# Performance work log

Hardware: AMD Instinct MI355X
Metric: run time of the kernel (lower is better)

Reference implementation:

```python
import jax, jax.numpy as jnp
import numpy as np

BS, SL, N_AGENTS, OBS_DIM, STATE_DIM, N_EDGES, HID = 32, 512, 32, 96, 1024, 64, 256


def _hgcn(w_line, x, H):
    # x: [B, n, 1]; H: [B, n, E]. Faithful to torch HGCN:
    # A = D^{-1/2} H |W| B^{-1} H^T D^{-1/2}, with D, B built from detached H/|W|,
    # inf entries (from 0^{-1} / 0^{-0.5}) zeroed. Diagonal matmuls are implicit scalings.
    w_abs = jnp.abs(w_line)
    Hd = jax.lax.stop_gradient(H)
    d = jnp.einsum('bne,e->bn', Hd, jax.lax.stop_gradient(w_abs))  # [B, n]
    d_is = jnp.where(d > 0, jax.lax.rsqrt(jnp.where(d > 0, d, 1.0)), 0.0)
    b = jnp.sum(Hd, axis=-2)  # [B, E]
    b_inv = jnp.where(b > 0, 1.0 / jnp.where(b > 0, b, 1.0), 0.0)
    t = d_is[..., None] * x                       # D^{-1/2} x
    s = jnp.einsum('bne,bnk->bek', H, t)          # H^T (...)
    s = s * (w_abs[None, :] * b_inv)[..., None]   # |W| B^{-1} (diagonals commute)
    y = jnp.einsum('bne,bek->bnk', H, s)          # H (...)
    return d_is[..., None] * y                    # D^{-1/2} (...)


def _mlp(x, w1, b1, w2, b2):
    return jax.nn.relu(x @ w1 + b1) @ w2 + b2


def setup_inputs() -> dict:
    key = jax.random.key(0)
    ks = jax.random.split(key, 24)
    f = jax.random.normal
    inp = {
        'agent_qs': f(ks[0], (BS, SL, N_AGENTS), jnp.float32),
        'states': f(ks[1], (BS, SL, STATE_DIM), jnp.float32),
        'indiv_us': f(ks[2], (BS, SL, N_AGENTS, OBS_DIM), jnp.float32),
        'edge_W': f(ks[3], (OBS_DIM, N_EDGES), jnp.float32) * 0.1,
        'edge_b': f(ks[4], (N_EDGES,), jnp.float32) * 0.1,
        'wline1': 1.0 + 0.1 * f(ks[5], (N_EDGES,), jnp.float32),
        'wline2': 1.0 + 0.1 * f(ks[6], (N_EDGES,), jnp.float32),
    }
    names = ['hw1', 'hc1', 'hw', 'hc']
    outs = [N_AGENTS, N_AGENTS, N_AGENTS, 1]
    for i, (nm, od) in enumerate(zip(names, outs)):
        inp[nm + '_w1'] = f(ks[7 + 4 * i], (STATE_DIM, HID), jnp.float32) * 0.05
        inp[nm + '_b1'] = f(ks[8 + 4 * i], (HID,), jnp.float32) * 0.05
        inp[nm + '_w2'] = f(ks[9 + 4 * i], (HID, od), jnp.float32) * 0.05
        inp[nm + '_b2'] = f(ks[10 + 4 * i], (od,), jnp.float32) * 0.05
    return inp


def reference(agent_qs, states, indiv_us, edge_W, edge_b, wline1, wline2,
              hw1_w1, hw1_b1, hw1_w2, hw1_b2, hc1_w1, hc1_b1, hc1_w2, hc1_b2,
              hw_w1, hw_b1, hw_w2, hw_b2, hc_w1, hc_b1, hc_w2, hc_b2):
    bs, sl, n = agent_qs.shape
    q = agent_qs.reshape(-1, n)                               # [B, n]
    u = indiv_us.reshape(-1, n, indiv_us.shape[-1])           # [B, n, obs]
    s = states.reshape(-1, states.shape[-1])                  # [B, state_dim]
    H = jax.nn.relu(u @ edge_W + edge_b)                      # hyper_edge_net -> [B, n, E]
    x = q[..., None]                                          # node_features [B, n, 1]
    qs_tot = _hgcn(wline2, _hgcn(wline1, x, H), H)[..., 0]    # two stacked HGCN encoders
    w1 = jnp.abs(_mlp(s, hw1_w1, hw1_b1, hw1_w2, hw1_b2))
    c1 = _mlp(s, hc1_w1, hc1_b1, hc1_w2, hc1_b2)
    qt = jax.nn.elu(qs_tot * w1 + c1)
    w = jnp.abs(_mlp(s, hw_w1, hw_b1, hw_w2, hw_b2))
    c = _mlp(s, hc_w1, hc_b1, hc_w2, hc_b2)[..., 0]
    q_tot = jnp.sum(qt * w, axis=-1) + c
    return q_tot.reshape(bs, sl, 1)
```

## Files before the change

### kernel.cpp

```cpp
#include <hip/hip_runtime.h>
#include <cstdint>

typedef _Float16 f16;
typedef _Float16 f16x2 __attribute__((ext_vector_type(2)));
typedef _Float16 f16x4 __attribute__((ext_vector_type(4)));
typedef _Float16 f16x8 __attribute__((ext_vector_type(8)));
typedef float f32x4 __attribute__((ext_vector_type(4)));

#define AS1U const __attribute__((address_space(1))) unsigned int
#define AS3U __attribute__((address_space(3))) unsigned int

__device__ __forceinline__ void gload_lds16(const void* g, void* l) {
    __builtin_amdgcn_global_load_lds((AS1U*)g, (AS3U*)l, 16, 0, 0);
}

#define WSYNC() asm volatile("s_waitcnt lgkmcnt(0)" ::: "memory")

#define BATCH 16384
#define NAG   32
#define OBS   96
#define SDIM  1024
#define NE    64
#define HIDN  256
#define NH    1024

#define NB_ST 1024
#define NB_PW 256
#define NB_SM 101
#define NB_HG 4096
#define NB_FRONT (NB_ST + NB_PW + NB_SM + NB_HG)

__global__ __launch_bounds__(256) void k_front(
    const float* __restrict__ agent_qs, const float* __restrict__ states,
    const float* __restrict__ indiv_us, const float* __restrict__ edge_W,
    const float* __restrict__ edge_b, const float* __restrict__ wline1,
    const float* __restrict__ wline2,
    const float* __restrict__ w1a, const float* __restrict__ w1b,
    const float* __restrict__ w1c, const float* __restrict__ w1d,
    const float* __restrict__ b1a, const float* __restrict__ b1b,
    const float* __restrict__ b1c, const float* __restrict__ b1d,
    const float* __restrict__ w2a, const float* __restrict__ w2b,
    const float* __restrict__ w2c, const float* __restrict__ w2d,
    f16* __restrict__ states16, f16* __restrict__ W1t, float* __restrict__ b1cat,
    f16* __restrict__ W2t, f16* __restrict__ hcw2, float* __restrict__ qs_tot) {
    __shared__ __align__(16) char arena[34304];
    const int tid = threadIdx.x;
    int bid = blockIdx.x;

    if (bid < NB_ST) {
        int i = bid * 256 + tid;
        const int n4 = BATCH * SDIM / 4;
        const int stride = NB_ST * 256;
        for (; i < n4; i += stride) {
            float4 v = ((const float4*)states)[i];
            f16x4 h = { (f16)v.x, (f16)v.y, (f16)v.z, (f16)v.w };
            ((f16x4*)states16)[i] = h;
        }
        return;
    }
    bid -= NB_ST;
    if (bid < NB_PW) {
        float* tile = (float*)arena;
        int mlp = bid >> 6, rem = bid & 63, kt = rem >> 2, ct = rem & 3;
        const float* src = (mlp == 0) ? w1a : (mlp == 1) ? w1b : (mlp == 2) ? w1c : w1d;
        int k0 = kt * 64, c0 = ct * 64;
        for (int i = tid; i < 4096; i += 256) {
            int kk = i >> 6, cc = i & 63;
            tile[kk * 65 + cc] = src[(size_t)(k0 + kk) * 256 + c0 + cc];
        }
        __syncthreads();
        for (int i = tid; i < 4096; i += 256) {
            int cc = i >> 6, kk = i & 63;
            W1t[(size_t)(mlp * 256 + c0 + cc) * 1024 + k0 + kk] = (f16)tile[kk * 65 + cc];
        }
        return;
    }
    bid -= NB_PW;
    if (bid < NB_SM) {
        int i = bid * 256 + tid;
        if (i < 24576) {
            int mp = i >> 13, rem = i & 8191, oo = rem >> 8, kk = rem & 255;
            const float* src = (mp == 0) ? w2a : (mp == 1) ? w2b : w2c;
            W2t[i] = (f16)src[kk * 32 + oo];
        } else if (i < 24832) {
            int k = i - 24576;
            hcw2[k] = (f16)w2d[k];
        } else {
            int n = i - 24832;
            int mlp = n >> 8, c = n & 255;
            const float* bsrc = (mlp == 0) ? b1a : (mlp == 1) ? b1b : (mlp == 2) ? b1c : b1d;
            b1cat[n] = bsrc[c];
        }
        return;
    }
    bid -= NB_SM;

    f16*   eWs   = (f16*)arena;
    float* swa   = (float*)(arena + 13312);
    f16*   HsB   = (f16*)(arena + 13824);
    float* svB   = (float*)(arena + 30720);
    float* sttB  = (float*)(arena + 31744);
    float* sdisB = (float*)(arena + 32256);
    float* sbinvB= (float*)(arena + 33280);

    const int w = tid >> 6, l = tid & 63;
    const int b = bid * 4 + w;
    f16*   Hw    = HsB + w * (32 * 66);
    float* sv    = svB + w * 64;
    float* stt   = sttB + w * 32;
    float* sdis  = sdisB + w * 64;
    float* sbinv = sbinvB + w * 64;

    for (int i = tid; i < 6144; i += 256) {
        int k = i >> 6, n = i & 63;
        eWs[n * 104 + k] = (f16)edge_W[i];
    }
    if (tid < 64) swa[tid] = fabsf(wline1[tid]);
    else if (tid < 128) swa[tid] = fabsf(wline2[tid - 64]);
    __syncthreads();

    const int lm = l & 15, lk = l >> 4;
    const float* ub = indiv_us + (size_t)b * (NAG * OBS);

    #pragma unroll
    for (int mt = 0; mt < 2; mt++) {
        f16x8 af[3];
        #pragma unroll
        for (int ks = 0; ks < 3; ks++) {
            const float* up = ub + (mt * 16 + lm) * 96 + ks * 32 + lk * 8;
            float4 v0 = *(const float4*)up;
            float4 v1 = *(const float4*)(up + 4);
            af[ks] = (f16x8){ (f16)v0.x, (f16)v0.y, (f16)v0.z, (f16)v0.w,
                              (f16)v1.x, (f16)v1.y, (f16)v1.z, (f16)v1.w };
        }
        #pragma unroll
        for (int nt = 0; nt < 4; nt++) {
            f32x4 acc = {0.f, 0.f, 0.f, 0.f};
            #pragma unroll
            for (int ks = 0; ks < 3; ks++) {
                f16x8 bb = *(const f16x8*)&eWs[(nt * 16 + lm) * 104 + ks * 32 + lk * 8];
                acc = __builtin_amdgcn_mfma_f32_16x16x32_f16(af[ks], bb, acc, 0, 0, 0);
            }
            int col = nt * 16 + lm;
            float bias = edge_b[col];
            #pragma unroll
            for (int r = 0; r < 4; r++) {
                int row = mt * 16 + lk * 4 + r;
                float hv = acc[r] + bias;
                Hw[row * 66 + col] = (f16)(hv > 0.f ? hv : 0.f);
            }
        }
    }
    WSYNC();

    float bsum = 0.f;
    #pragma unroll
    for (int n = 0; n < 32; n++) bsum += (float)Hw[n * 66 + l];
    sbinv[l] = bsum > 0.f ? 1.f / bsum : 0.f;

    const int nn = l & 31, half = l >> 5;
    float dd = 0.f;
    #pragma unroll 8
    for (int e2 = 0; e2 < 32; e2++) {
        f16x2 h2 = *(const f16x2*)&Hw[nn * 66 + e2 * 2];
        dd += (float)h2.x * swa[half * 64 + e2 * 2] + (float)h2.y * swa[half * 64 + e2 * 2 + 1];
    }
    float dis = dd > 0.f ? rsqrtf(dd) : 0.f;
    sdis[l] = dis;
    float q = agent_qs[(size_t)b * 32 + nn];
    if (half == 0) stt[nn] = dis * q;
    WSYNC();

    float s1 = 0.f;
    #pragma unroll
    for (int n = 0; n < 32; n++) s1 += (float)Hw[n * 66 + l] * stt[n];
    sv[l] = s1 * swa[l] * sbinv[l];
    WSYNC();

    float y1 = 0.f;
    #pragma unroll 8
    for (int e2 = 0; e2 < 32; e2++) {
        f16x2 h2 = *(const f16x2*)&Hw[nn * 66 + e2 * 2];
        y1 += (float)h2.x * sv[e2 * 2] + (float)h2.y * sv[e2 * 2 + 1];
    }
    float x2 = sdis[nn] * y1;
    if (half == 0) stt[nn] = sdis[32 + nn] * x2;
    WSYNC();

    float s2 = 0.f;
    #pragma unroll
    for (int n = 0; n < 32; n++) s2 += (float)Hw[n * 66 + l] * stt[n];
    sv[l] = s2 * swa[64 + l] * sbinv[l];
    WSYNC();

    float y2 = 0.f;
    #pragma unroll 8
    for (int e2 = 0; e2 < 32; e2++) {
        f16x2 h2 = *(const f16x2*)&Hw[nn * 66 + e2 * 2];
        y2 += (float)h2.x * sv[e2 * 2] + (float)h2.y * sv[e2 * 2 + 1];
    }
    if (half == 0) qs_tot[(size_t)b * 32 + nn] = sdis[32 + nn] * y2;
}

__global__ __launch_bounds__(256) void k_gemm1(
    const f16* __restrict__ A, const f16* __restrict__ B,
    const float* __restrict__ b1cat, const f16* __restrict__ W2t,
    const f16* __restrict__ hcw2, float* __restrict__ Pp) {
    __shared__ __align__(16) char smem[33792];
    f16* As = (f16*)smem;
    f16* Bs = (f16*)(smem + 16384);
    f16* Ts = (f16*)smem;

    const int tid = threadIdx.x;
    const int w = tid >> 6, l = tid & 63;
    const int p = blockIdx.x;
    const int xcd = p & 7, slot = p >> 3;
    const int region = slot >> 6, rs = slot & 63;
    const int mt = (xcd * 2 + region) * 8 + (rs >> 3);
    const int nt = rs & 7;
    const int m0 = mt * 128, n0 = nt * 128;
    const int wm = w >> 1, wn = w & 1;
    const int lm = l & 15, lk = l >> 4;
    const int srow = l >> 3;
    const int scol = (l & 7) * 8;

    f32x4 acc[4][4];
    #pragma unroll
    for (int i = 0; i < 4; i++)
        #pragma unroll
        for (int j = 0; j < 4; j++) acc[i][j] = (f32x4){0.f, 0.f, 0.f, 0.f};

    for (int kt = 0; kt < 16; kt++) {
        #pragma unroll
        for (int i = 0; i < 4; i++) {
            int c = w * 4 + i;
            int row = c * 8 + srow;
            gload_lds16(&A[(size_t)(m0 + row) * 1024 + kt * 64 + scol], &As[c * 512]);
            gload_lds16(&B[(size_t)(n0 + row) * 1024 + kt * 64 + scol], &Bs[c * 512]);
        }
        __syncthreads();
        #pragma unroll
        for (int ks = 0; ks < 2; ks++) {
            f16x8 a[4], bb[4];
            #pragma unroll
            for (int i = 0; i < 4; i++)
                a[i] = *(const f16x8*)&As[(wm * 64 + i * 16 + lm) * 64 + ks * 32 + lk * 8];
            #pragma unroll
            for (int j = 0; j < 4; j++)
                bb[j] = *(const f16x8*)&Bs[(wn * 64 + j * 16 + lm) * 64 + ks * 32 + lk * 8];
            #pragma unroll
            for (int i = 0; i < 4; i++)
                #pragma unroll
                for (int j = 0; j < 4; j++)
                    acc[i][j] = __builtin_amdgcn_mfma_f32_16x16x32_f16(a[i], bb[j], acc[i][j], 0, 0, 0);
        }
        __syncthreads();
    }

    float bj[4];
    #pragma unroll
    for (int j = 0; j < 4; j++) bj[j] = b1cat[n0 + wn * 64 + j * 16 + lm];
    #pragma unroll
    for (int i = 0; i < 4; i++)
        #pragma unroll
        for (int r = 0; r < 4; r++) {
            int row = wm * 64 + i * 16 + lk * 4 + r;
            #pragma unroll
            for (int j = 0; j < 4; j++) {
                int col = wn * 64 + j * 16 + lm;
                float v = acc[i][j][r] + bj[j];
                Ts[row * 132 + col] = (f16)(v > 0.f ? v : 0.f);
            }
        }
    __syncthreads();

    const int mlp = nt >> 1, kh = nt & 1;
    const int rbase = w * 32;
    if (mlp < 3) {
        const f16* wb = W2t + mlp * 8192 + kh * 128;
        f32x4 acc2[2][2];
        acc2[0][0] = (f32x4){0,0,0,0}; acc2[0][1] = (f32x4){0,0,0,0};
        acc2[1][0] = (f32x4){0,0,0,0}; acc2[1][1] = (f32x4){0,0,0,0};
        #pragma unroll
        for (int ks = 0; ks < 4; ks++) {
            f16x8 b0 = *(const f16x8*)&wb[lm * 256 + ks * 32 + lk * 8];
            f16x8 b1 = *(const f16x8*)&wb[(16 + lm) * 256 + ks * 32 + lk * 8];
            #pragma unroll
            for (int i2 = 0; i2 < 2; i2++) {
                f16x8 a = *(const f16x8*)&Ts[(rbase + i2 * 16 + lm) * 132 + ks * 32 + lk * 8];
                acc2[i2][0] = __builtin_amdgcn_mfma_f32_16x16x32_f16(a, b0, acc2[i2][0], 0, 0, 0);
                acc2[i2][1] = __builtin_amdgcn_mfma_f32_16x16x32_f16(a, b1, acc2[i2][1], 0, 0, 0);
            }
        }
        #pragma unroll
        for (int i2 = 0; i2 < 2; i2++)
            #pragma unroll
            for (int j2 = 0; j2 < 2; j2++)
                #pragma unroll
                for (int r = 0; r < 4; r++)
                    Pp[((size_t)kh * BATCH + m0 + rbase + i2 * 16 + lk * 4 + r) * 104
                       + mlp * 32 + j2 * 16 + lm] = acc2[i2][j2][r];
    } else {
        const f16* hc = hcw2 + kh * 128;
        f32x4 acc2[2];
        acc2[0] = (f32x4){0,0,0,0}; acc2[1] = (f32x4){0,0,0,0};
        #pragma unroll
        for (int ks = 0; ks < 4; ks++) {
            f16x8 bz = (f16x8){0,0,0,0,0,0,0,0};
            if (lm == 0) bz = *(const f16x8*)&hc[ks * 32 + lk * 8];
            #pragma unroll
            for (int i2 = 0; i2 < 2; i2++) {
                f16x8 a = *(const f16x8*)&Ts[(rbase + i2 * 16 + lm) * 132 + ks * 32 + lk * 8];
                acc2[i2] = __builtin_amdgcn_mfma_f32_16x16x32_f16(a, bz, acc2[i2], 0, 0, 0);
            }
        }
        if (lm == 0)
            #pragma unroll
            for (int i2 = 0; i2 < 2; i2++)
                #pragma unroll
                for (int r = 0; r < 4; r++)
                    Pp[((size_t)kh * BATCH + m0 + rbase + i2 * 16 + lk * 4 + r) * 104 + 96]
                        = acc2[i2][r];
    }
}

__global__ __launch_bounds__(256) void k_ep(
    const float* __restrict__ Pp, const float* __restrict__ qs_tot,
    const float* __restrict__ hw1_b2, const float* __restrict__ hc1_b2,
    const float* __restrict__ hw_b2, const float* __restrict__ hc_b2,
    float* __restrict__ out) {
    const int tid = threadIdx.x;
    const int row = blockIdx.x * 32 + (tid >> 3);
    const int q8 = tid & 7, o = q8 * 4;
    const float* p0 = Pp + (size_t)row * 104;
    const float* p1 = Pp + (size_t)(BATCH + row) * 104;
    f32x4 a0 = *(const f32x4*)(p0 + o);
    f32x4 a1 = *(const f32x4*)(p1 + o);
    f32x4 c0 = *(const f32x4*)(p0 + 32 + o);
    f32x4 c1 = *(const f32x4*)(p1 + 32 + o);
    f32x4 w0 = *(const f32x4*)(p0 + 64 + o);
    f32x4 w1 = *(const f32x4*)(p1 + 64 + o);
    f32x4 qs = *(const f32x4*)(qs_tot + (size_t)row * 32 + o);
    float val = 0.f;
    #pragma unroll
    for (int j = 0; j < 4; j++) {
        float wv1 = fabsf(a0[j] + a1[j] + hw1_b2[o + j]);
        float cv1 = c0[j] + c1[j] + hc1_b2[o + j];
        float wv  = fabsf(w0[j] + w1[j] + hw_b2[o + j]);
        float z = qs[j] * wv1 + cv1;
        float qt = z > 0.f ? z : expm1f(z);
        val += qt * wv;
    }
    val += __shfl_xor(val, 1);
    val += __shfl_xor(val, 2);
    val += __shfl_xor(val, 4);
    if (q8 == 0) out[row] = val + p0[96] + p1[96] + hc_b2[0];
}

extern "C" void kernel_launch(void* const* d_in, const int* in_sizes, int n_in,
                              void* d_out, int out_size, void* d_ws, size_t ws_size,
                              hipStream_t stream) {
    const float* agent_qs = (const float*)d_in[0];
    const float* states   = (const float*)d_in[1];
    const float* indiv_us = (const float*)d_in[2];
    const float* edge_W   = (const float*)d_in[3];
    const float* edge_b   = (const float*)d_in[4];
    const float* wline1   = (const float*)d_in[5];
    const float* wline2   = (const float*)d_in[6];
    const float* hw1_w1 = (const float*)d_in[7];
    const float* hw1_b1 = (const float*)d_in[8];
    const float* hw1_w2 = (const float*)d_in[9];
    const float* hw1_b2 = (const float*)d_in[10];
    const float* hc1_w1 = (const float*)d_in[11];
    const float* hc1_b1 = (const float*)d_in[12];
    const float* hc1_w2 = (const float*)d_in[13];
    const float* hc1_b2 = (const float*)d_in[14];
    const float* hw_w1  = (const float*)d_in[15];
    const float* hw_b1  = (const float*)d_in[16];
    const float* hw_w2  = (const float*)d_in[17];
    const float* hw_b2  = (const float*)d_in[18];
    const float* hc_w1  = (const float*)d_in[19];
    const float* hc_b1  = (const float*)d_in[20];
    const float* hc_w2  = (const float*)d_in[21];
    const float* hc_b2  = (const float*)d_in[22];

    char* ws = (char*)d_ws;
    size_t o_states16 = 0;
    size_t o_qs   = o_states16 + (size_t)BATCH * SDIM * 2;
    size_t o_W1t  = o_qs + (size_t)BATCH * NAG * 4;
    size_t o_b1   = o_W1t + (size_t)NH * SDIM * 2;
    size_t o_W2t  = o_b1 + 4096;
    size_t o_hcw2 = o_W2t + 49152;
    size_t o_Pp   = o_hcw2 + 512;

    f16*   states16 = (f16*)(ws + o_states16);
    float* qs_tot   = (float*)(ws + o_qs);
    f16*   W1t      = (f16*)(ws + o_W1t);
    float* b1cat    = (float*)(ws + o_b1);
    f16*   W2t      = (f16*)(ws + o_W2t);
    f16*   hcw2     = (f16*)(ws + o_hcw2);
    float* Pp       = (float*)(ws + o_Pp);

    k_front<<<NB_FRONT, 256, 0, stream>>>(
        agent_qs, states, indiv_us, edge_W, edge_b, wline1, wline2,
        hw1_w1, hc1_w1, hw_w1, hc_w1, hw1_b1, hc1_b1, hw_b1, hc_b1,
        hw1_w2, hc1_w2, hw_w2, hc_w2,
        states16, W1t, b1cat, W2t, hcw2, qs_tot);
    k_gemm1<<<1024, 256, 0, stream>>>(states16, W1t, b1cat, W2t, hcw2, Pp);
    k_ep<<<BATCH / 32, 256, 0, stream>>>(Pp, qs_tot, hw1_b2, hc1_b2, hw_b2, hc_b2,
                                         (float*)d_out);
}
```

Before: 138.0 us.

## Move HGCN computation from front kernel into the epilogue kernel

The hypergraph convolution work moves out of the front prep kernel and into the final epilogue kernel, which now computes qs_tot per batch row and combines it directly with the MLP outputs. This removes the qs_tot round trip through global memory and shrinks the front kernel's LDS footprint, which helps occupancy of its conversion blocks. The fused kernel stores intermediate LDS vectors in fp16 and sets a launch-bounds occupancy hint. The cost is lower precision for the HGCN scalars, and the HGCN work now runs after the GEMM instead of alongside the front-stage conversion blocks.

```diff
diff --git a/kernel.cpp b/kernel.cpp
--- a/kernel.cpp
+++ b/kernel.cpp
@@ -27,14 +27,10 @@
 #define NB_ST 1024
 #define NB_PW 256
 #define NB_SM 101
-#define NB_HG 4096
-#define NB_FRONT (NB_ST + NB_PW + NB_SM + NB_HG)
+#define NB_FRONT (NB_ST + NB_PW + NB_SM)
 
 __global__ __launch_bounds__(256) void k_front(
-    const float* __restrict__ agent_qs, const float* __restrict__ states,
-    const float* __restrict__ indiv_us, const float* __restrict__ edge_W,
-    const float* __restrict__ edge_b, const float* __restrict__ wline1,
-    const float* __restrict__ wline2,
+    const float* __restrict__ states,
     const float* __restrict__ w1a, const float* __restrict__ w1b,
     const float* __restrict__ w1c, const float* __restrict__ w1d,
     const float* __restrict__ b1a, const float* __restrict__ b1b,
@@ -42,8 +38,8 @@
     const float* __restrict__ w2a, const float* __restrict__ w2b,
     const float* __restrict__ w2c, const float* __restrict__ w2d,
     f16* __restrict__ states16, f16* __restrict__ W1t, float* __restrict__ b1cat,
-    f16* __restrict__ W2t, f16* __restrict__ hcw2, float* __restrict__ qs_tot) {
-    __shared__ __align__(16) char arena[34304];
+    f16* __restrict__ W2t, f16* __restrict__ hcw2) {
+    __shared__ float tile[64 * 65];
     const int tid = threadIdx.x;
     int bid = blockIdx.x;
 
@@ -60,7 +56,6 @@
     }
     bid -= NB_ST;
     if (bid < NB_PW) {
-        float* tile = (float*)arena;
         int mlp = bid >> 6, rem = bid & 63, kt = rem >> 2, ct = rem & 3;
         const float* src = (mlp == 0) ? w1a : (mlp == 1) ? w1b : (mlp == 2) ? w1c : w1d;
         int k0 = kt * 64, c0 = ct * 64;
@@ -76,7 +71,7 @@
         return;
     }
     bid -= NB_PW;
-    if (bid < NB_SM) {
+    {
         int i = bid * 256 + tid;
         if (i < 24576) {
             int mp = i >> 13, rem = i & 8191, oo = rem >> 8, kk = rem & 255;
@@ -85,121 +80,13 @@
         } else if (i < 24832) {
             int k = i - 24576;
             hcw2[k] = (f16)w2d[k];
-        } else {
+        } else if (i < 25856) {
             int n = i - 24832;
             int mlp = n >> 8, c = n & 255;
             const float* bsrc = (mlp == 0) ? b1a : (mlp == 1) ? b1b : (mlp == 2) ? b1c : b1d;
             b1cat[n] = bsrc[c];
         }
-        return;
-    }
-    bid -= NB_SM;
-
-    f16*   eWs   = (f16*)arena;
-    float* swa   = (float*)(arena + 13312);
-    f16*   HsB   = (f16*)(arena + 13824);
-    float* svB   = (float*)(arena + 30720);
-    float* sttB  = (float*)(arena + 31744);
-    float* sdisB = (float*)(arena + 32256);
-    float* sbinvB= (float*)(arena + 33280);
-
-    const int w = tid >> 6, l = tid & 63;
-    const int b = bid * 4 + w;
-    f16*   Hw    = HsB + w * (32 * 66);
-    float* sv    = svB + w * 64;
-    float* stt   = sttB + w * 32;
-    float* sdis  = sdisB + w * 64;
-    float* sbinv = sbinvB + w * 64;
-
-    for (int i = tid; i < 6144; i += 256) {
-        int k = i >> 6, n = i & 63;
-        eWs[n * 104 + k] = (f16)edge_W[i];
-    }
-    if (tid < 64) swa[tid] = fabsf(wline1[tid]);
-    else if (tid < 128) swa[tid] = fabsf(wline2[tid - 64]);
-    __syncthreads();
-
-    const int lm = l & 15, lk = l >> 4;
-    const float* ub = indiv_us + (size_t)b * (NAG * OBS);
-
-    #pragma unroll
-    for (int mt = 0; mt < 2; mt++) {
-        f16x8 af[3];
-        #pragma unroll
-        for (int ks = 0; ks < 3; ks++) {
-            const float* up = ub + (mt * 16 + lm) * 96 + ks * 32 + lk * 8;
-            float4 v0 = *(const float4*)up;
-            float4 v1 = *(const float4*)(up + 4);
-            af[ks] = (f16x8){ (f16)v0.x, (f16)v0.y, (f16)v0.z, (f16)v0.w,
-                              (f16)v1.x, (f16)v1.y, (f16)v1.z, (f16)v1.w };
-        }
-        #pragma unroll
-        for (int nt = 0; nt < 4; nt++) {
-            f32x4 acc = {0.f, 0.f, 0.f, 0.f};
-            #pragma unroll
-            for (int ks = 0; ks < 3; ks++) {
-                f16x8 bb = *(const f16x8*)&eWs[(nt * 16 + lm) * 104 + ks * 32 + lk * 8];
-                acc = __builtin_amdgcn_mfma_f32_16x16x32_f16(af[ks], bb, acc, 0, 0, 0);
-            }
-            int col = nt * 16 + lm;
-            float bias = edge_b[col];
-            #pragma unroll
-            for (int r = 0; r < 4; r++) {
-                int row = mt * 16 + lk * 4 + r;
-                float hv = acc[r] + bias;
-                Hw[row * 66 + col] = (f16)(hv > 0.f ? hv : 0.f);
-            }
-        }
-    }
-    WSYNC();
-
-    float bsum = 0.f;
-    #pragma unroll
-    for (int n = 0; n < 32; n++) bsum += (float)Hw[n * 66 + l];
-    sbinv[l] = bsum > 0.f ? 1.f / bsum : 0.f;
-
-    const int nn = l & 31, half = l >> 5;
-    float dd = 0.f;
-    #pragma unroll 8
-    for (int e2 = 0; e2 < 32; e2++) {
-        f16x2 h2 = *(const f16x2*)&Hw[nn * 66 + e2 * 2];
-        dd += (float)h2.x * swa[half * 64 + e2 * 2] + (float)h2.y * swa[half * 64 + e2 * 2 + 1];
-    }
-    float dis = dd > 0.f ? rsqrtf(dd) : 0.f;
-    sdis[l] = dis;
-    float q = agent_qs[(size_t)b * 32 + nn];
-    if (half == 0) stt[nn] = dis * q;
-    WSYNC();
-
-    float s1 = 0.f;
-    #pragma unroll
-    for (int n = 0; n < 32; n++) s1 += (float)Hw[n * 66 + l] * stt[n];
-    sv[l] = s1 * swa[l] * sbinv[l];
-    WSYNC();
-
-    float y1 = 0.f;
-    #pragma unroll 8
-    for (int e2 = 0; e2 < 32; e2++) {
-        f16x2 h2 = *(const f16x2*)&Hw[nn * 66 + e2 * 2];
-        y1 += (float)h2.x * sv[e2 * 2] + (float)h2.y * sv[e2 * 2 + 1];
-    }
-    float x2 = sdis[nn] * y1;
-    if (half == 0) stt[nn] = sdis[32 + nn] * x2;
-    WSYNC();
-
-    float s2 = 0.f;
-    #pragma unroll
-    for (int n = 0; n < 32; n++) s2 += (float)Hw[n * 66 + l] * stt[n];
-    sv[l] = s2 * swa[64 + l] * sbinv[l];
-    WSYNC();
-
-    float y2 = 0.f;
-    #pragma unroll 8
-    for (int e2 = 0; e2 < 32; e2++) {
-        f16x2 h2 = *(const f16x2*)&Hw[nn * 66 + e2 * 2];
-        y2 += (float)h2.x * sv[e2 * 2] + (float)h2.y * sv[e2 * 2 + 1];
-    }
-    if (half == 0) qs_tot[(size_t)b * 32 + nn] = sdis[32 + nn] * y2;
+    }
 }
 
 __global__ __launch_bounds__(256) void k_gemm1(
@@ -324,37 +211,150 @@
     }
 }
 
-__global__ __launch_bounds__(256) void k_ep(
-    const float* __restrict__ Pp, const float* __restrict__ qs_tot,
+__global__ __launch_bounds__(256, 5) void k_hgcn_ep(
+    const float* __restrict__ agent_qs, const float* __restrict__ indiv_us,
+    const float* __restrict__ edge_W, const float* __restrict__ edge_b,
+    const float* __restrict__ wline1, const float* __restrict__ wline2,
+    const float* __restrict__ Pp,
     const float* __restrict__ hw1_b2, const float* __restrict__ hc1_b2,
     const float* __restrict__ hw_b2, const float* __restrict__ hc_b2,
     float* __restrict__ out) {
+    __shared__ __align__(16) char arena[32512];
+    f16*   eWs   = (f16*)arena;
+    float* swa   = (float*)(arena + 13312);
+    f16*   HsB   = (f16*)(arena + 13824);
+    f16*   svB   = (f16*)(arena + 30720);
+    f16*   sttB  = (f16*)(arena + 31232);
+    f16*   sdisB = (f16*)(arena + 31488);
+    f16*   sbinvB= (f16*)(arena + 32000);
+
     const int tid = threadIdx.x;
-    const int row = blockIdx.x * 32 + (tid >> 3);
-    const int q8 = tid & 7, o = q8 * 4;
-    const float* p0 = Pp + (size_t)row * 104;
-    const float* p1 = Pp + (size_t)(BATCH + row) * 104;
-    f32x4 a0 = *(const f32x4*)(p0 + o);
-    f32x4 a1 = *(const f32x4*)(p1 + o);
-    f32x4 c0 = *(const f32x4*)(p0 + 32 + o);
-    f32x4 c1 = *(const f32x4*)(p1 + 32 + o);
-    f32x4 w0 = *(const f32x4*)(p0 + 64 + o);
-    f32x4 w1 = *(const f32x4*)(p1 + 64 + o);
-    f32x4 qs = *(const f32x4*)(qs_tot + (size_t)row * 32 + o);
-    float val = 0.f;
-    #pragma unroll
-    for (int j = 0; j < 4; j++) {
-        float wv1 = fabsf(a0[j] + a1[j] + hw1_b2[o + j]);
-        float cv1 = c0[j] + c1[j] + hc1_b2[o + j];
-        float wv  = fabsf(w0[j] + w1[j] + hw_b2[o + j]);
-        float z = qs[j] * wv1 + cv1;
-        float qt = z > 0.f ? z : expm1f(z);
-        val += qt * wv;
-    }
-    val += __shfl_xor(val, 1);
-    val += __shfl_xor(val, 2);
-    val += __shfl_xor(val, 4);
-    if (q8 == 0) out[row] = val + p0[96] + p1[96] + hc_b2[0];
+    const int w = tid >> 6, l = tid & 63;
+    const int b = blockIdx.x * 4 + w;
+    f16* Hw    = HsB + w * (32 * 66);
+    f16* sv    = svB + w * 64;
+    f16* stt   = sttB + w * 32;
+    f16* sdis  = sdisB + w * 64;
+    f16* sbinv = sbinvB + w * 64;
+
+    const int nn = l & 31, half = l >> 5;
+
+    float pa0 = 0.f, pa1 = 0.f, pc0 = 0.f, pc1 = 0.f, pw0 = 0.f, pw1 = 0.f;
+    float p96a = 0.f, p96b = 0.f, bw1 = 0.f, bc1 = 0.f, bww = 0.f, bhc = 0.f;
+    if (half == 0) {
+        const float* p0 = Pp + (size_t)b * 104;
+        const float* p1 = Pp + (size_t)(BATCH + b) * 104;
+        pa0 = p0[nn];      pa1 = p1[nn];
+        pc0 = p0[32 + nn]; pc1 = p1[32 + nn];
+        pw0 = p0[64 + nn]; pw1 = p1[64 + nn];
+        p96a = p0[96];     p96b = p1[96];
+        bw1 = hw1_b2[nn];  bc1 = hc1_b2[nn];
+        bww = hw_b2[nn];   bhc = hc_b2[0];
+    }
+    float q = agent_qs[(size_t)b * 32 + nn];
+
+    for (int i = tid; i < 6144; i += 256) {
+        int k = i >> 6, n = i & 63;
+        eWs[n * 104 + k] = (f16)edge_W[i];
+    }
+    if (tid < 64) swa[tid] = fabsf(wline1[tid]);
+    else if (tid < 128) swa[tid] = fabsf(wline2[tid - 64]);
+    __syncthreads();
+
+    const int lm = l & 15, lk = l >> 4;
+    const float* ub = indiv_us + (size_t)b * (NAG * OBS);
+
+    #pragma unroll
+    for (int mt = 0; mt < 2; mt++) {
+        f16x8 af[3];
+        #pragma unroll
+        for (int ks = 0; ks < 3; ks++) {
+            const float* up = ub + (mt * 16 + lm) * 96 + ks * 32 + lk * 8;
+            float4 v0 = *(const float4*)up;
+            float4 v1 = *(const float4*)(up + 4);
+            af[ks] = (f16x8){ (f16)v0.x, (f16)v0.y, (f16)v0.z, (f16)v0.w,
+                              (f16)v1.x, (f16)v1.y, (f16)v1.z, (f16)v1.w };
+        }
+        #pragma unroll
+        for (int nt = 0; nt < 4; nt++) {
+            f32x4 acc = {0.f, 0.f, 0.f, 0.f};
+            #pragma unroll
+            for (int ks = 0; ks < 3; ks++) {
+                f16x8 bb = *(const f16x8*)&eWs[(nt * 16 + lm) * 104 + ks * 32 + lk * 8];
+                acc = __builtin_amdgcn_mfma_f32_16x16x32_f16(af[ks], bb, acc, 0, 0, 0);
+            }
+            int col = nt * 16 + lm;
+            float bias = edge_b[col];
+            #pragma unroll
+            for (int r = 0; r < 4; r++) {
+                int row = mt * 16 + lk * 4 + r;
+                float hv = acc[r] + bias;
+                Hw[row * 66 + col] = (f16)(hv > 0.f ? hv : 0.f);
+            }
+        }
+    }
+    WSYNC();
+
+    float bsum = 0.f;
+    #pragma unroll
+    for (int n = 0; n < 32; n++) bsum += (float)Hw[n * 66 + l];
+    sbinv[l] = (f16)(bsum > 0.f ? 1.f / bsum : 0.f);
+
+    float dd = 0.f;
+    #pragma unroll 8
+    for (int e2 = 0; e2 < 32; e2++) {
+        f16x2 h2 = *(const f16x2*)&Hw[nn * 66 + e2 * 2];
+        dd += (float)h2.x * swa[half * 64 + e2 * 2] + (float)h2.y * swa[half * 64 + e2 * 2 + 1];
+    }
+    float dis = dd > 0.f ? rsqrtf(dd) : 0.f;
+    sdis[l] = (f16)dis;
+    if (half == 0) stt[nn] = (f16)(dis * q);
+    WSYNC();
+
+    float s1 = 0.f;
+    #pragma unroll
+    for (int n = 0; n < 32; n++) s1 += (float)Hw[n * 66 + l] * (float)stt[n];
+    sv[l] = (f16)(s1 * swa[l] * (float)sbinv[l]);
+    WSYNC();
+
+    float y1 = 0.f;
+    #pragma unroll 8
+    for (int e2 = 0; e2 < 32; e2++) {
+        f16x2 h2 = *(const f16x2*)&Hw[nn * 66 + e2 * 2];
+        f16x2 s2v = *(const f16x2*)&sv[e2 * 2];
+        y1 += (float)h2.x * (float)s2v.x + (float)h2.y * (float)s2v.y;
+    }
+    float x2 = (float)sdis[nn] * y1;
+    if (half == 0) stt[nn] = (f16)((float)sdis[32 + nn] * x2);
+    WSYNC();
+
+    float s2 = 0.f;
+    #pragma unroll
+    for (int n = 0; n < 32; n++) s2 += (float)Hw[n * 66 + l] * (float)stt[n];
+    sv[l] = (f16)(s2 * swa[64 + l] * (float)sbinv[l]);
+    WSYNC();
+
+    float y2 = 0.f;
+    #pragma unroll 8
+    for (int e2 = 0; e2 < 32; e2++) {
+        f16x2 h2 = *(const f16x2*)&Hw[nn * 66 + e2 * 2];
+        f16x2 s2v = *(const f16x2*)&sv[e2 * 2];
+        y2 += (float)h2.x * (float)s2v.x + (float)h2.y * (float)s2v.y;
+    }
+
+    float qsv = (float)sdis[32 + nn] * y2;
+    float w1v = fabsf(pa0 + pa1 + bw1);
+    float c1v = pc0 + pc1 + bc1;
+    float wwv = fabsf(pw0 + pw1 + bww);
+    float z = qsv * w1v + c1v;
+    float qt = z > 0.f ? z : expm1f(z);
+    float val = (half == 0) ? qt * wwv : 0.f;
+    val += __shfl_xor(val, 1, 32);
+    val += __shfl_xor(val, 2, 32);
+    val += __shfl_xor(val, 4, 32);
+    val += __shfl_xor(val, 8, 32);
+    val += __shfl_xor(val, 16, 32);
+    if (l == 0) out[b] = val + p96a + p96b + bhc;
 }
 
 extern "C" void kernel_launch(void* const* d_in, const int* in_sizes, int n_in,
@@ -386,15 +386,13 @@
 
     char* ws = (char*)d_ws;
     size_t o_states16 = 0;
-    size_t o_qs   = o_states16 + (size_t)BATCH * SDIM * 2;
-    size_t o_W1t  = o_qs + (size_t)BATCH * NAG * 4;
+    size_t o_W1t  = o_states16 + (size_t)BATCH * SDIM * 2;
     size_t o_b1   = o_W1t + (size_t)NH * SDIM * 2;
     size_t o_W2t  = o_b1 + 4096;
     size_t o_hcw2 = o_W2t + 49152;
     size_t o_Pp   = o_hcw2 + 512;
 
     f16*   states16 = (f16*)(ws + o_states16);
-    float* qs_tot   = (float*)(ws + o_qs);
     f16*   W1t      = (f16*)(ws + o_W1t);
     float* b1cat    = (float*)(ws + o_b1);
     f16*   W2t      = (f16*)(ws + o_W2t);
@@ -402,11 +400,12 @@
     float* Pp       = (float*)(ws + o_Pp);
 
     k_front<<<NB_FRONT, 256, 0, stream>>>(
-        agent_qs, states, indiv_us, edge_W, edge_b, wline1, wline2,
+        states,
         hw1_w1, hc1_w1, hw_w1, hc_w1, hw1_b1, hc1_b1, hw_b1, hc_b1,
         hw1_w2, hc1_w2, hw_w2, hc_w2,
-        states16, W1t, b1cat, W2t, hcw2, qs_tot);
+        states16, W1t, b1cat, W2t, hcw2);
     k_gemm1<<<1024, 256, 0, stream>>>(states16, W1t, b1cat, W2t, hcw2, Pp);
-    k_ep<<<BATCH / 32, 256, 0, stream>>>(Pp, qs_tot, hw1_b2, hc1_b2, hw_b2, hc_b2,
-                                         (float*)d_out);
+    k_hgcn_ep<<<BATCH / 4, 256, 0, stream>>>(
+        agent_qs, indiv_us, edge_W, edge_b, wline1, wline2, Pp,
+        hw1_b2, hc1_b2, hw_b2, hc_b2, (float*)d_out);
 }
```

New measurement: 136.5 us. About the same (-1.1%).
